# Kernel tuning notes

Hardware: AMD Instinct MI355X
Metric: run time of the kernel (lower is better)

Reference implementation:

```python
import jax, jax.numpy as jnp
import numpy as np

# Circuit geometry (matches QNN(sequence_length=16384, quantum_layer_quantity=4, output_quantity=64, entangler='basic'))
SEQ_LEN = 16384
N_ADDR = 14                      # ceil(log2(16384))
N_DATA = 4                       # UNIQUE_NUCLEOTIDE_QUANTITY
N_WIRES = N_ADDR + N_DATA        # 18
DIM = 2 ** N_WIRES               # 262144
N_LAYERS = 4
OUT = 64
BATCH = 32


def _apply_rx(state, theta, w):
    """Apply RX(theta) on wire w (wire 0 = most significant bit)."""
    c = jnp.cos(theta / 2).astype(jnp.complex64)
    s = (-1j * jnp.sin(theta / 2)).astype(jnp.complex64)
    U = jnp.stack([jnp.stack([c, s]), jnp.stack([s, c])])  # [2,2]
    B = state.shape[0]
    st = state.reshape(B, 2 ** w, 2, -1)
    st = jnp.einsum('ij,bajc->baic', U, st)
    return st.reshape(B, DIM)


def _apply_cnot(state, c, t):
    """CNOT with control wire c, target wire t."""
    B = state.shape[0]
    st = state.reshape((B,) + (2,) * N_WIRES)
    c_ax, t_ax = 1 + c, 1 + t
    p0 = jnp.take(st, 0, axis=c_ax)
    p1 = jnp.take(st, 1, axis=c_ax)
    t_ax_r = t_ax - 1 if t_ax > c_ax else t_ax
    p1 = jnp.flip(p1, axis=t_ax_r)  # X on target within control=1 block
    st = jnp.stack([p0, p1], axis=c_ax)
    return st.reshape(B, DIM)


def _circuit_probs(x, qweights):
    # Encoding: address register stays |0...0>, so among all multi-controlled
    # BasisEmbeddings only index 0 (control pattern all zeros) applies its X
    # gates. Resulting basis state index = bits of x[:,0,:] on the 4 data
    # wires (least-significant bits), address bits = 0.
    bits = x[:, 0, :]  # [B, 4]
    pw = jnp.asarray([8, 4, 2, 1], dtype=jnp.int32)
    idx = jnp.sum(bits * pw, axis=-1)  # [B]
    state = jax.nn.one_hot(idx, DIM, dtype=jnp.complex64)  # [B, DIM]
    # BasicEntanglerLayers: per layer, RX on every wire then a CNOT ring.
    for l in range(N_LAYERS):
        for w in range(N_WIRES):
            state = _apply_rx(state, qweights[l, w], w)
        for w in range(N_WIRES):
            state = _apply_cnot(state, w, (w + 1) % N_WIRES)
    return jnp.abs(state) ** 2  # qml.probs over all wires -> [B, DIM] float32


def setup_inputs() -> dict:
    key = jax.random.key(0)
    kx, kw, kW = jax.random.split(key, 3)
    x = jax.random.randint(kx, (BATCH, SEQ_LEN, N_DATA), 0, 2, dtype=jnp.int32)
    qweights = jax.random.uniform(kw, (N_LAYERS, N_WIRES), dtype=jnp.float32,
                                  maxval=2.0 * np.pi)
    W = jax.random.normal(kW, (OUT, DIM), dtype=jnp.float32) / np.sqrt(DIM)
    b = jnp.zeros((OUT,), dtype=jnp.float32)
    return {"x": x, "qweights": qweights, "W": W, "b": b}


def reference(x, qweights, W, b):
    probs = _circuit_probs(x, qweights)          # [B, 2^18]
    logits = probs @ W.T + b                     # [B, 64]
    return jax.nn.sigmoid(logits)
```

## Files before the change

kernel.cpp:

```cpp
#include <hip/hip_runtime.h>
#include <math.h>


#define DIM (1 << 18)
#define NW 18
#define CH 128
#define CPB 2
#define NMM (DIM / (CH * CPB))

#define PAD16(i) ((i) + ((i) >> 4))

typedef short short8 __attribute__((ext_vector_type(8)));
typedef float f32x4  __attribute__((ext_vector_type(4)));

__device__ __forceinline__ unsigned perm18(unsigned i) {
    unsigned s = i;
    s ^= s >> 1; s ^= s >> 2; s ^= s >> 4; s ^= s >> 8; s ^= s >> 16;
    unsigned out = s & 0x1FFFFu;
    out |= ((s ^ (i >> 17)) & 1u) << 17;
    return out;
}

__device__ __forceinline__ unsigned pinv18(unsigned b) {
    unsigned t = b & 0x1FFFFu;
    unsigned u = (t ^ (t >> 1)) & 0xFFFFu;
    unsigned i17 = ((b >> 17) ^ t) & 1u;
    unsigned i16 = ((t >> 16) ^ i17) & 1u;
    return u | (i16 << 16) | (i17 << 17);
}

__device__ __forceinline__ void bfly(float2& a0, float2& a1, float c, float s) {
    float2 n0 = make_float2(c * a0.x + s * a1.y, c * a0.y - s * a1.x);
    float2 n1 = make_float2(c * a1.x + s * a0.y, c * a1.y - s * a0.x);
    a0 = n0; a1 = n1;
}

__device__ __forceinline__ short f2bf(float x) {
    unsigned u = __float_as_uint(x);
    return (short)((u + 0x7FFFu + ((u >> 16) & 1u)) >> 16);
}

template<int R>
__device__ __forceinline__ void ldsRound(float2* t, int m, const float2* gsh) {
    constexpr int B = 1 << (2 * R);
    int low = m & (B - 1);
    int high = m >> (2 * R);
    int ib = (high << (2 * R + 2)) | low;
    int p00 = PAD16(ib), p01 = PAD16(ib | B), p10 = PAD16(ib | (2 * B)), p11 = PAD16(ib | (3 * B));
    float2 e00 = t[p00], e01 = t[p01], e10 = t[p10], e11 = t[p11];
    float2 g0 = gsh[2 * R], g1 = gsh[2 * R + 1];
    bfly(e00, e01, g0.x, g0.y);
    bfly(e10, e11, g0.x, g0.y);
    bfly(e00, e10, g1.x, g1.y);
    bfly(e01, e11, g1.x, g1.y);
    t[p00] = e00; t[p01] = e01; t[p10] = e10; t[p11] = e11;
}

__global__ __launch_bounds__(256) void kInit(float2* buf, const float* qw) {
    __shared__ float2 t[1088];
    __shared__ float2 gsh[10];
    int tid = threadIdx.x;
    if (tid < 10) {
        float th = qw[1 * NW + (17 - tid)] * 0.5f;
        gsh[tid] = make_float2(cosf(th), sinf(th));
    }
    float c[NW], s[NW];
#pragma unroll
    for (int w = 0; w < NW; ++w) {
        float th = qw[w] * 0.5f;
        c[w] = cosf(th); s[w] = sinf(th);
    }
    unsigned base = blockIdx.x * 1024u;
    float2 e[4];
#pragma unroll
    for (int b = 0; b < 4; ++b) {
        unsigned i = pinv18(base + 4 * tid + b);
        float m = 1.0f;
#pragma unroll
        for (int p = 0; p < 18; ++p)
            m *= ((i >> p) & 1u) ? s[17 - p] : c[17 - p];
        int k4 = __popc(i) & 3;
        if      (k4 == 0) e[b] = make_float2( m, 0.f);
        else if (k4 == 1) e[b] = make_float2(0.f, -m);
        else if (k4 == 2) e[b] = make_float2(-m, 0.f);
        else              e[b] = make_float2(0.f,  m);
    }
    __syncthreads();
    bfly(e[0], e[1], gsh[0].x, gsh[0].y);
    bfly(e[2], e[3], gsh[0].x, gsh[0].y);
    bfly(e[0], e[2], gsh[1].x, gsh[1].y);
    bfly(e[1], e[3], gsh[1].x, gsh[1].y);
    int ib = 4 * tid;
    t[PAD16(ib)] = e[0]; t[PAD16(ib + 1)] = e[1]; t[PAD16(ib + 2)] = e[2]; t[PAD16(ib + 3)] = e[3];
    __syncthreads();
    ldsRound<1>(t, tid, gsh); __syncthreads();
    ldsRound<2>(t, tid, gsh); __syncthreads();
    ldsRound<3>(t, tid, gsh); __syncthreads();
    float2 f00 = t[PAD16(tid)], f01 = t[PAD16(tid + 256)];
    float2 f10 = t[PAD16(tid + 512)], f11 = t[PAD16(tid + 768)];
    bfly(f00, f01, gsh[8].x, gsh[8].y);
    bfly(f10, f11, gsh[8].x, gsh[8].y);
    bfly(f00, f10, gsh[9].x, gsh[9].y);
    bfly(f01, f11, gsh[9].x, gsh[9].y);
    buf[base + tid] = f00; buf[base + tid + 256] = f01;
    buf[base + tid + 512] = f10; buf[base + tid + 768] = f11;
}

__global__ __launch_bounds__(256) void kA(float2* buf, const float* qw, int layer) {
    __shared__ float2 t[1088];
    __shared__ float2 gsh[10];
    int tid = threadIdx.x;
    if (tid < 10) {
        float th = qw[layer * NW + (17 - tid)] * 0.5f;
        gsh[tid] = make_float2(cosf(th), sinf(th));
    }
    unsigned base = blockIdx.x * 1024u;
    float2 e0 = buf[base + 4 * tid + 0];
    float2 e1 = buf[base + 4 * tid + 1];
    float2 e2 = buf[base + 4 * tid + 2];
    float2 e3 = buf[base + 4 * tid + 3];
    __syncthreads();
    bfly(e0, e1, gsh[0].x, gsh[0].y);
    bfly(e2, e3, gsh[0].x, gsh[0].y);
    bfly(e0, e2, gsh[1].x, gsh[1].y);
    bfly(e1, e3, gsh[1].x, gsh[1].y);
    int ib = 4 * tid;
    t[PAD16(ib)] = e0; t[PAD16(ib + 1)] = e1; t[PAD16(ib + 2)] = e2; t[PAD16(ib + 3)] = e3;
    __syncthreads();
    ldsRound<1>(t, tid, gsh); __syncthreads();
    ldsRound<2>(t, tid, gsh); __syncthreads();
    ldsRound<3>(t, tid, gsh); __syncthreads();
    float2 f00 = t[PAD16(tid)], f01 = t[PAD16(tid + 256)];
    float2 f10 = t[PAD16(tid + 512)], f11 = t[PAD16(tid + 768)];
    bfly(f00, f01, gsh[8].x, gsh[8].y);
    bfly(f10, f11, gsh[8].x, gsh[8].y);
    bfly(f00, f10, gsh[9].x, gsh[9].y);
    bfly(f01, f11, gsh[9].x, gsh[9].y);
    buf[base + tid] = f00; buf[base + tid + 256] = f01;
    buf[base + tid + 512] = f10; buf[base + tid + 768] = f11;
}

__global__ __launch_bounds__(256) void kBC(const float2* __restrict__ in, float2* out,
                                           float* probs, const float* qw, int layer) {
    __shared__ float2 t[1088];
    __shared__ float2 gsh[8];
    int tid = threadIdx.x;
    if (tid < 8) {
        float th = qw[layer * NW + (7 - tid)] * 0.5f;
        gsh[tid] = make_float2(cosf(th), sinf(th));
    }
    unsigned mblk = blockIdx.x;
    int mh = tid >> 2, lo = tid & 3;
    unsigned ibase = (mblk << 2) | lo;
    float2 e0 = in[((unsigned)(4 * mh + 0) << 10) | ibase];
    float2 e1 = in[((unsigned)(4 * mh + 1) << 10) | ibase];
    float2 e2 = in[((unsigned)(4 * mh + 2) << 10) | ibase];
    float2 e3 = in[((unsigned)(4 * mh + 3) << 10) | ibase];
    __syncthreads();
    bfly(e0, e1, gsh[0].x, gsh[0].y);
    bfly(e2, e3, gsh[0].x, gsh[0].y);
    bfly(e0, e2, gsh[1].x, gsh[1].y);
    bfly(e1, e3, gsh[1].x, gsh[1].y);
    {
        int k = 4 * (4 * mh) + lo;
        t[PAD16(k)] = e0; t[PAD16(k + 4)] = e1; t[PAD16(k + 8)] = e2; t[PAD16(k + 12)] = e3;
    }
    __syncthreads();
    {
        int hb = ((mh >> 2) << 4) | (mh & 3);
        int k00 = 4 * hb + lo, k01 = 4 * (hb | 4) + lo, k10 = 4 * (hb | 8) + lo, k11 = 4 * (hb | 12) + lo;
        int p00 = PAD16(k00), p01 = PAD16(k01), p10 = PAD16(k10), p11 = PAD16(k11);
        float2 a0 = t[p00], a1 = t[p01], a2 = t[p10], a3 = t[p11];
        bfly(a0, a1, gsh[2].x, gsh[2].y);
        bfly(a2, a3, gsh[2].x, gsh[2].y);
        bfly(a0, a2, gsh[3].x, gsh[3].y);
        bfly(a1, a3, gsh[3].x, gsh[3].y);
        t[p00] = a0; t[p01] = a1; t[p10] = a2; t[p11] = a3;
    }
    __syncthreads();
    {
        int hb = ((mh >> 4) << 6) | (mh & 15);
        int k00 = 4 * hb + lo, k01 = 4 * (hb | 16) + lo, k10 = 4 * (hb | 32) + lo, k11 = 4 * (hb | 48) + lo;
        int p00 = PAD16(k00), p01 = PAD16(k01), p10 = PAD16(k10), p11 = PAD16(k11);
        float2 a0 = t[p00], a1 = t[p01], a2 = t[p10], a3 = t[p11];
        bfly(a0, a1, gsh[4].x, gsh[4].y);
        bfly(a2, a3, gsh[4].x, gsh[4].y);
        bfly(a0, a2, gsh[5].x, gsh[5].y);
        bfly(a1, a3, gsh[5].x, gsh[5].y);
        t[p00] = a0; t[p01] = a1; t[p10] = a2; t[p11] = a3;
    }
    __syncthreads();
    {
        int k = 4 * mh + lo;
        float2 a0 = t[PAD16(k)], a1 = t[PAD16(k + 256)], a2 = t[PAD16(k + 512)], a3 = t[PAD16(k + 768)];
        bfly(a0, a1, gsh[6].x, gsh[6].y);
        bfly(a2, a3, gsh[6].x, gsh[6].y);
        bfly(a0, a2, gsh[7].x, gsh[7].y);
        bfly(a1, a3, gsh[7].x, gsh[7].y);
        unsigned i0 = ((unsigned)(mh +   0) << 10) | ibase;
        unsigned i1 = ((unsigned)(mh +  64) << 10) | ibase;
        unsigned i2 = ((unsigned)(mh + 128) << 10) | ibase;
        unsigned i3 = ((unsigned)(mh + 192) << 10) | ibase;
        if (probs) {
            probs[perm18(i0)] = a0.x * a0.x + a0.y * a0.y;
            probs[perm18(i1)] = a1.x * a1.x + a1.y * a1.y;
            probs[perm18(i2)] = a2.x * a2.x + a2.y * a2.y;
            probs[perm18(i3)] = a3.x * a3.x + a3.y * a3.y;
        } else {
            out[perm18(i0)] = a0;
            out[perm18(i1)] = a1;
            out[perm18(i2)] = a2;
            out[perm18(i3)] = a3;
        }
    }
}

__global__ __launch_bounds__(256) void k_mm(const float* __restrict__ p0,
                                            const float* __restrict__ W,
                                            float* __restrict__ partial) {
    __shared__ short Wl[64][136];
    __shared__ short Pl[16][136];
    __shared__ unsigned Tsh[16];
    int tid = threadIdx.x;
    if (tid < 16) {
        unsigned v = (unsigned)tid;
#pragma unroll
        for (int r = 0; r < 4; ++r) v = perm18(v);
        Tsh[tid] = v;
    }
    __syncthreads();

    unsigned d00 = (unsigned)blockIdx.x * (CH * CPB);
    int wrow = tid >> 5;
    int wcol = (tid & 31) * 4;
    int prow = tid >> 7;
    int pcol = tid & 127;
    unsigned Tp[8];
#pragma unroll
    for (int t = 0; t < 8; ++t) Tp[t] = Tsh[prow + 2 * t];

    int lane = tid & 63, wv = tid >> 6;
    f32x4 acc = {0.f, 0.f, 0.f, 0.f};

    float4 wr[8];
    float  pr[8];

#pragma unroll
    for (int t = 0; t < 8; ++t)
        wr[t] = *(const float4*)&W[(size_t)(wrow + 8 * t) * DIM + d00 + wcol];
#pragma unroll
    for (int t = 0; t < 8; ++t)
        pr[t] = p0[(d00 ^ (Tp[t] & ~127u)) + pcol];
#pragma unroll
    for (int t = 0; t < 8; ++t) {
        short4 b = make_short4(f2bf(wr[t].x), f2bf(wr[t].y), f2bf(wr[t].z), f2bf(wr[t].w));
        *(short4*)&Wl[wrow + 8 * t][wcol] = b;
    }
#pragma unroll
    for (int t = 0; t < 8; ++t)
        Pl[prow + 2 * t][pcol ^ (Tp[t] & 127u)] = f2bf(pr[t]);
    __syncthreads();

    {
        unsigned d1 = d00 + CH;
#pragma unroll
        for (int t = 0; t < 8; ++t)
            wr[t] = *(const float4*)&W[(size_t)(wrow + 8 * t) * DIM + d1 + wcol];
#pragma unroll
        for (int t = 0; t < 8; ++t)
            pr[t] = p0[(d1 ^ (Tp[t] & ~127u)) + pcol];
    }

    int arow = lane & 15, kg = (lane >> 4) * 8;
#pragma unroll
    for (int kk = 0; kk < 4; ++kk) {
        short8 a = *(const short8*)&Pl[arow][kk * 32 + kg];
        short8 b = *(const short8*)&Wl[16 * wv + arow][kk * 32 + kg];
        acc = __builtin_amdgcn_mfma_f32_16x16x32_bf16(a, b, acc, 0, 0, 0);
    }
    __syncthreads();

#pragma unroll
    for (int t = 0; t < 8; ++t) {
        short4 b = make_short4(f2bf(wr[t].x), f2bf(wr[t].y), f2bf(wr[t].z), f2bf(wr[t].w));
        *(short4*)&Wl[wrow + 8 * t][wcol] = b;
    }
#pragma unroll
    for (int t = 0; t < 8; ++t)
        Pl[prow + 2 * t][pcol ^ (Tp[t] & 127u)] = f2bf(pr[t]);
    __syncthreads();

#pragma unroll
    for (int kk = 0; kk < 4; ++kk) {
        short8 a = *(const short8*)&Pl[arow][kk * 32 + kg];
        short8 b = *(const short8*)&Wl[16 * wv + arow][kk * 32 + kg];
        acc = __builtin_amdgcn_mfma_f32_16x16x32_bf16(a, b, acc, 0, 0, 0);
    }

    float* dst = partial + (size_t)blockIdx.x * 1024;
#pragma unroll
    for (int r = 0; r < 4; ++r) {
        int jrow = (lane >> 4) * 4 + r;
        dst[jrow * 64 + 16 * wv + (lane & 15)] = acc[r];
    }
}

__global__ __launch_bounds__(256) void k_finalize(const float* __restrict__ partial,
                                                  const float* __restrict__ bias,
                                                  const int* __restrict__ x,
                                                  float* __restrict__ out) {
    int b = blockIdx.x;
    int tid = threadIdx.x;
    int ji = tid & 15, ci = tid >> 4;
    int jo = b * 16 + ji;
    float sum = 0.f;
#pragma unroll 8
    for (int c = ci; c < NMM; c += 16)
        sum += partial[(size_t)c * 1024 + jo];
    __shared__ float red[16][17];
    __shared__ float lg[16];
    __shared__ int sidx[32];
    red[ci][ji] = sum;
    if (tid < 32) {
        const int* xb = x + (size_t)tid * (16384 * 4);
        sidx[tid] = 8 * xb[0] + 4 * xb[1] + 2 * xb[2] + xb[3];
    }
    __syncthreads();
    if (ci == 0) {
        float s = 0.f;
#pragma unroll
        for (int k = 0; k < 16; ++k) s += red[k][ji];
        lg[ji] = s + bias[jo & 63];
    }
    __syncthreads();
    int myidx = b >> 2, o0 = (b & 3) * 16;
#pragma unroll
    for (int r = 0; r < 2; ++r) {
        int slot = tid + 256 * r;
        int bb = slot >> 4, k = slot & 15;
        if (sidx[bb] == myidx) {
            float z = lg[k];
            out[bb * 64 + o0 + k] = 1.f / (1.f + expf(-z));
        }
    }
}

extern "C" void kernel_launch(void* const* d_in, const int* in_sizes, int n_in,
                              void* d_out, int out_size, void* d_ws, size_t ws_size,
                              hipStream_t stream) {
    const int*   x    = (const int*)d_in[0];
    const float* qw   = (const float*)d_in[1];
    const float* W    = (const float*)d_in[2];
    const float* bias = (const float*)d_in[3];
    float* out = (float*)d_out;

    char* ws = (char*)d_ws;
    float2*   buf0    = (float2*)(ws + (1ull << 20));
    float2*   buf1    = (float2*)(ws + (4ull << 20));
    float*    probs   = (float*)(ws + (8ull << 20));
    float*    partial = (float*)(ws + (16ull << 20));

    kInit<<<256, 256, 0, stream>>>(buf0, qw);
    kBC  <<<256, 256, 0, stream>>>(buf0, buf1, nullptr, qw, 1);
    kA   <<<256, 256, 0, stream>>>(buf1, qw, 2);
    kBC  <<<256, 256, 0, stream>>>(buf1, buf0, nullptr, qw, 2);
    kA   <<<256, 256, 0, stream>>>(buf0, qw, 3);
    kBC  <<<256, 256, 0, stream>>>(buf0, nullptr, probs, qw, 3);

    k_mm<<<NMM, 256, 0, stream>>>(probs, W, partial);
    k_finalize<<<64, 256, 0, stream>>>(partial, bias, x, out);
}
```

Before: 57.39 us.

## Repartition state-vector butterfly passes and lengthen matmul chunk loop

Changes how qubit wires are split between the A and B/C passes. The A kernels now handle wires 0 and 17 plus the wires selected by the block index, and perform the CNOT-ring permutation while gathering into shared memory. The B/C kernel becomes an in-place pass with plain strided stores, and the probability scatter through perm18 happens only in the last pass. The matmul kernel now processes 4 chunks per block in a prefetch loop instead of 2, which halves the block count and the partial-sum traffic but leaves fewer blocks to fill the GPU.

```diff
diff --git a/kernel.cpp b/kernel.cpp
--- a/kernel.cpp
+++ b/kernel.cpp
@@ -5,7 +5,7 @@
 #define DIM (1 << 18)
 #define NW 18
 #define CH 128
-#define CPB 2
+#define CPB 4
 #define NMM (DIM / (CH * CPB))
 
 #define PAD16(i) ((i) + ((i) >> 4))
@@ -29,6 +29,11 @@
     return u | (i16 << 16) | (i17 << 17);
 }
 
+__device__ __forceinline__ unsigned ginv9(unsigned x) {
+    x ^= x >> 1; x ^= x >> 2; x ^= x >> 4; x ^= x >> 8;
+    return x & 511u;
+}
+
 __device__ __forceinline__ void bfly(float2& a0, float2& a1, float c, float s) {
     float2 n0 = make_float2(c * a0.x + s * a1.y, c * a0.y - s * a1.x);
     float2 n1 = make_float2(c * a1.x + s * a0.y, c * a1.y - s * a0.x);
@@ -40,15 +45,14 @@
     return (short)((u + 0x7FFFu + ((u >> 16) & 1u)) >> 16);
 }
 
-template<int R>
-__device__ __forceinline__ void ldsRound(float2* t, int m, const float2* gsh) {
-    constexpr int B = 1 << (2 * R);
+template<int RB>
+__device__ __forceinline__ void slotRound(float2* t, int m, float2 g0, float2 g1) {
+    constexpr int B = 1 << RB;
     int low = m & (B - 1);
-    int high = m >> (2 * R);
-    int ib = (high << (2 * R + 2)) | low;
-    int p00 = PAD16(ib), p01 = PAD16(ib | B), p10 = PAD16(ib | (2 * B)), p11 = PAD16(ib | (3 * B));
+    int high = m >> RB;
+    int ib = (high << (RB + 2)) | low;
+    int p00 = PAD16(ib), p01 = PAD16(ib | B), p10 = PAD16(ib | 2 * B), p11 = PAD16(ib | 3 * B);
     float2 e00 = t[p00], e01 = t[p01], e10 = t[p10], e11 = t[p11];
-    float2 g0 = gsh[2 * R], g1 = gsh[2 * R + 1];
     bfly(e00, e01, g0.x, g0.y);
     bfly(e10, e11, g0.x, g0.y);
     bfly(e00, e10, g1.x, g1.y);
@@ -56,12 +60,30 @@
     t[p00] = e00; t[p01] = e01; t[p10] = e10; t[p11] = e11;
 }
 
-__global__ __launch_bounds__(256) void kInit(float2* buf, const float* qw) {
+__device__ __forceinline__ void kaTail(float2* t, int tid, const float2* gsh,
+                                       float2* __restrict__ out, unsigned B9) {
+    slotRound<1>(t, tid, gsh[1], gsh[2]); __syncthreads();
+    slotRound<3>(t, tid, gsh[3], gsh[4]); __syncthreads();
+    slotRound<5>(t, tid, gsh[5], gsh[6]); __syncthreads();
+    int low = tid & 127, high = tid >> 7;
+    int ib = (high << 9) | low;
+    float2 a0 = t[PAD16(ib)], a1 = t[PAD16(ib | 128)];
+    float2 a2 = t[PAD16(ib | 256)], a3 = t[PAD16(ib | 384)];
+    bfly(a0, a1, gsh[7].x, gsh[7].y);
+    bfly(a2, a3, gsh[7].x, gsh[7].y);
+    bfly(a0, a2, gsh[8].x, gsh[8].y);
+    bfly(a1, a3, gsh[8].x, gsh[8].y);
+    unsigned ob = ((unsigned)high << 17) | (B9 << 9) | (unsigned)low;
+    out[ob] = a0; out[ob + 128] = a1; out[ob + 256] = a2; out[ob + 384] = a3;
+}
+
+__global__ __launch_bounds__(256) void kInit(float2* __restrict__ out, const float* qw) {
     __shared__ float2 t[1088];
     __shared__ float2 gsh[10];
     int tid = threadIdx.x;
     if (tid < 10) {
-        float th = qw[1 * NW + (17 - tid)] * 0.5f;
+        int p = (tid == 9) ? 17 : tid;
+        float th = qw[1 * NW + (17 - p)] * 0.5f;
         gsh[tid] = make_float2(cosf(th), sinf(th));
     }
     float c[NW], s[NW];
@@ -70,97 +92,105 @@
         float th = qw[w] * 0.5f;
         c[w] = cosf(th); s[w] = sinf(th);
     }
-    unsigned base = blockIdx.x * 1024u;
-    float2 e[4];
-#pragma unroll
-    for (int b = 0; b < 4; ++b) {
-        unsigned i = pinv18(base + 4 * tid + b);
-        float m = 1.0f;
-#pragma unroll
-        for (int p = 0; p < 18; ++p)
-            m *= ((i >> p) & 1u) ? s[17 - p] : c[17 - p];
-        int k4 = __popc(i) & 3;
-        if      (k4 == 0) e[b] = make_float2( m, 0.f);
-        else if (k4 == 1) e[b] = make_float2(0.f, -m);
-        else if (k4 == 2) e[b] = make_float2(-m, 0.f);
-        else              e[b] = make_float2(0.f,  m);
-    }
-    __syncthreads();
-    bfly(e[0], e[1], gsh[0].x, gsh[0].y);
-    bfly(e[2], e[3], gsh[0].x, gsh[0].y);
-    bfly(e[0], e[2], gsh[1].x, gsh[1].y);
-    bfly(e[1], e[3], gsh[1].x, gsh[1].y);
-    int ib = 4 * tid;
-    t[PAD16(ib)] = e[0]; t[PAD16(ib + 1)] = e[1]; t[PAD16(ib + 2)] = e[2]; t[PAD16(ib + 3)] = e[3];
-    __syncthreads();
-    ldsRound<1>(t, tid, gsh); __syncthreads();
-    ldsRound<2>(t, tid, gsh); __syncthreads();
-    ldsRound<3>(t, tid, gsh); __syncthreads();
-    float2 f00 = t[PAD16(tid)], f01 = t[PAD16(tid + 256)];
-    float2 f10 = t[PAD16(tid + 512)], f11 = t[PAD16(tid + 768)];
-    bfly(f00, f01, gsh[8].x, gsh[8].y);
-    bfly(f10, f11, gsh[8].x, gsh[8].y);
-    bfly(f00, f10, gsh[9].x, gsh[9].y);
-    bfly(f01, f11, gsh[9].x, gsh[9].y);
-    buf[base + tid] = f00; buf[base + tid + 256] = f01;
-    buf[base + tid + 512] = f10; buf[base + tid + 768] = f11;
-}
-
-__global__ __launch_bounds__(256) void kA(float2* buf, const float* qw, int layer) {
+    unsigned B9 = blockIdx.x;
+    float2 e[2][2];
+#pragma unroll
+    for (int p17 = 0; p17 < 2; ++p17)
+#pragma unroll
+        for (int b0 = 0; b0 < 2; ++b0) {
+            unsigned b = ((unsigned)p17 << 17) | (B9 << 9) | ((unsigned)tid << 1) | (unsigned)b0;
+            unsigned i = pinv18(b);
+            float m = 1.0f;
+#pragma unroll
+            for (int p = 0; p < 18; ++p)
+                m *= ((i >> p) & 1u) ? s[17 - p] : c[17 - p];
+            int k4 = __popc(i) & 3;
+            if      (k4 == 0) e[p17][b0] = make_float2( m, 0.f);
+            else if (k4 == 1) e[p17][b0] = make_float2(0.f, -m);
+            else if (k4 == 2) e[p17][b0] = make_float2(-m, 0.f);
+            else              e[p17][b0] = make_float2(0.f,  m);
+        }
+    __syncthreads();
+    bfly(e[0][0], e[0][1], gsh[0].x, gsh[0].y);
+    bfly(e[1][0], e[1][1], gsh[0].x, gsh[0].y);
+    bfly(e[0][0], e[1][0], gsh[9].x, gsh[9].y);
+    bfly(e[0][1], e[1][1], gsh[9].x, gsh[9].y);
+    int sb = tid << 1;
+    t[PAD16(sb)] = e[0][0];       t[PAD16(sb | 1)] = e[0][1];
+    t[PAD16(sb | 512)] = e[1][0]; t[PAD16(sb | 513)] = e[1][1];
+    __syncthreads();
+    kaTail(t, tid, gsh, out, B9);
+}
+
+__global__ __launch_bounds__(256) void kA(const float2* __restrict__ in,
+                                          float2* __restrict__ out,
+                                          const float* qw, int layer) {
     __shared__ float2 t[1088];
     __shared__ float2 gsh[10];
     int tid = threadIdx.x;
     if (tid < 10) {
-        float th = qw[layer * NW + (17 - tid)] * 0.5f;
+        int p = (tid == 9) ? 17 : tid;
+        float th = qw[layer * NW + (17 - p)] * 0.5f;
         gsh[tid] = make_float2(cosf(th), sinf(th));
     }
-    unsigned base = blockIdx.x * 1024u;
-    float2 e0 = buf[base + 4 * tid + 0];
-    float2 e1 = buf[base + 4 * tid + 1];
-    float2 e2 = buf[base + 4 * tid + 2];
-    float2 e3 = buf[base + 4 * tid + 3];
+    unsigned B9 = blockIdx.x;
+    unsigned C = pinv18(B9 << 9);
+    unsigned c9 = C & 511u;
+    unsigned base0 = C & ~511u;
+    unsigned base1 = base0 ^ 0x30000u;
+    float2 v[2][2];
+#pragma unroll
+    for (int ee = 0; ee < 2; ++ee)
+#pragma unroll
+        for (int r = 0; r < 2; ++r)
+            v[ee][r] = in[(ee ? base1 : base0) + (unsigned)tid + 256u * r];
+#pragma unroll
+    for (int ee = 0; ee < 2; ++ee)
+#pragma unroll
+        for (int r = 0; r < 2; ++r) {
+            unsigned k = (unsigned)tid + 256u * r;
+            unsigned x = (k ^ c9) & 511u;
+            unsigned bl = ginv9(x);
+            unsigned p17 = ((unsigned)__popc(x) ^ (unsigned)ee) & 1u;
+            t[PAD16((p17 << 9) | bl)] = v[ee][r];
+        }
+    __syncthreads();
+    {
+        int s00 = tid << 1;
+        int p00 = PAD16(s00), p01 = PAD16(s00 | 1), p10 = PAD16(s00 | 512), p11 = PAD16(s00 | 513);
+        float2 e00 = t[p00], e01 = t[p01], e10 = t[p10], e11 = t[p11];
+        bfly(e00, e01, gsh[0].x, gsh[0].y);
+        bfly(e10, e11, gsh[0].x, gsh[0].y);
+        bfly(e00, e10, gsh[9].x, gsh[9].y);
+        bfly(e01, e11, gsh[9].x, gsh[9].y);
+        t[p00] = e00; t[p01] = e01; t[p10] = e10; t[p11] = e11;
+    }
+    __syncthreads();
+    kaTail(t, tid, gsh, out, B9);
+}
+
+__global__ __launch_bounds__(256) void kBC(float2* __restrict__ buf, float* probs,
+                                           const float* qw, int layer) {
+    __shared__ float2 t[1088];
+    __shared__ float2 gsh[8];
+    int tid = threadIdx.x;
+    if (tid < 8) {
+        float th = qw[layer * NW + (8 - tid)] * 0.5f;
+        gsh[tid] = make_float2(cosf(th), sinf(th));
+    }
+    unsigned blk = blockIdx.x;
+    unsigned ibase = ((blk >> 7) << 17) | ((blk & 127u) << 2) | 0u;
+    int mh = tid >> 2, lo = tid & 3;
+    ibase |= (unsigned)lo;
+    float2 e0 = buf[((unsigned)(4 * mh + 0) << 9) | ibase];
+    float2 e1 = buf[((unsigned)(4 * mh + 1) << 9) | ibase];
+    float2 e2 = buf[((unsigned)(4 * mh + 2) << 9) | ibase];
+    float2 e3 = buf[((unsigned)(4 * mh + 3) << 9) | ibase];
     __syncthreads();
     bfly(e0, e1, gsh[0].x, gsh[0].y);
     bfly(e2, e3, gsh[0].x, gsh[0].y);
     bfly(e0, e2, gsh[1].x, gsh[1].y);
     bfly(e1, e3, gsh[1].x, gsh[1].y);
-    int ib = 4 * tid;
-    t[PAD16(ib)] = e0; t[PAD16(ib + 1)] = e1; t[PAD16(ib + 2)] = e2; t[PAD16(ib + 3)] = e3;
-    __syncthreads();
-    ldsRound<1>(t, tid, gsh); __syncthreads();
-    ldsRound<2>(t, tid, gsh); __syncthreads();
-    ldsRound<3>(t, tid, gsh); __syncthreads();
-    float2 f00 = t[PAD16(tid)], f01 = t[PAD16(tid + 256)];
-    float2 f10 = t[PAD16(tid + 512)], f11 = t[PAD16(tid + 768)];
-    bfly(f00, f01, gsh[8].x, gsh[8].y);
-    bfly(f10, f11, gsh[8].x, gsh[8].y);
-    bfly(f00, f10, gsh[9].x, gsh[9].y);
-    bfly(f01, f11, gsh[9].x, gsh[9].y);
-    buf[base + tid] = f00; buf[base + tid + 256] = f01;
-    buf[base + tid + 512] = f10; buf[base + tid + 768] = f11;
-}
-
-__global__ __launch_bounds__(256) void kBC(const float2* __restrict__ in, float2* out,
-                                           float* probs, const float* qw, int layer) {
-    __shared__ float2 t[1088];
-    __shared__ float2 gsh[8];
-    int tid = threadIdx.x;
-    if (tid < 8) {
-        float th = qw[layer * NW + (7 - tid)] * 0.5f;
-        gsh[tid] = make_float2(cosf(th), sinf(th));
-    }
-    unsigned mblk = blockIdx.x;
-    int mh = tid >> 2, lo = tid & 3;
-    unsigned ibase = (mblk << 2) | lo;
-    float2 e0 = in[((unsigned)(4 * mh + 0) << 10) | ibase];
-    float2 e1 = in[((unsigned)(4 * mh + 1) << 10) | ibase];
-    float2 e2 = in[((unsigned)(4 * mh + 2) << 10) | ibase];
-    float2 e3 = in[((unsigned)(4 * mh + 3) << 10) | ibase];
-    __syncthreads();
-    bfly(e0, e1, gsh[0].x, gsh[0].y);
-    bfly(e2, e3, gsh[0].x, gsh[0].y);
-    bfly(e0, e2, gsh[1].x, gsh[1].y);
-    bfly(e1, e3, gsh[1].x, gsh[1].y);
     {
         int k = 4 * (4 * mh) + lo;
         t[PAD16(k)] = e0; t[PAD16(k + 4)] = e1; t[PAD16(k + 8)] = e2; t[PAD16(k + 12)] = e3;
@@ -168,8 +198,8 @@
     __syncthreads();
     {
         int hb = ((mh >> 2) << 4) | (mh & 3);
-        int k00 = 4 * hb + lo, k01 = 4 * (hb | 4) + lo, k10 = 4 * (hb | 8) + lo, k11 = 4 * (hb | 12) + lo;
-        int p00 = PAD16(k00), p01 = PAD16(k01), p10 = PAD16(k10), p11 = PAD16(k11);
+        int p00 = PAD16(4 * hb + lo), p01 = PAD16(4 * (hb | 4) + lo);
+        int p10 = PAD16(4 * (hb | 8) + lo), p11 = PAD16(4 * (hb | 12) + lo);
         float2 a0 = t[p00], a1 = t[p01], a2 = t[p10], a3 = t[p11];
         bfly(a0, a1, gsh[2].x, gsh[2].y);
         bfly(a2, a3, gsh[2].x, gsh[2].y);
@@ -180,8 +210,8 @@
     __syncthreads();
     {
         int hb = ((mh >> 4) << 6) | (mh & 15);
-        int k00 = 4 * hb + lo, k01 = 4 * (hb | 16) + lo, k10 = 4 * (hb | 32) + lo, k11 = 4 * (hb | 48) + lo;
-        int p00 = PAD16(k00), p01 = PAD16(k01), p10 = PAD16(k10), p11 = PAD16(k11);
+        int p00 = PAD16(4 * hb + lo), p01 = PAD16(4 * (hb | 16) + lo);
+        int p10 = PAD16(4 * (hb | 32) + lo), p11 = PAD16(4 * (hb | 48) + lo);
         float2 a0 = t[p00], a1 = t[p01], a2 = t[p10], a3 = t[p11];
         bfly(a0, a1, gsh[4].x, gsh[4].y);
         bfly(a2, a3, gsh[4].x, gsh[4].y);
@@ -197,20 +227,17 @@
         bfly(a2, a3, gsh[6].x, gsh[6].y);
         bfly(a0, a2, gsh[7].x, gsh[7].y);
         bfly(a1, a3, gsh[7].x, gsh[7].y);
-        unsigned i0 = ((unsigned)(mh +   0) << 10) | ibase;
-        unsigned i1 = ((unsigned)(mh +  64) << 10) | ibase;
-        unsigned i2 = ((unsigned)(mh + 128) << 10) | ibase;
-        unsigned i3 = ((unsigned)(mh + 192) << 10) | ibase;
+        unsigned i0 = ((unsigned)(mh +   0) << 9) | ibase;
+        unsigned i1 = ((unsigned)(mh +  64) << 9) | ibase;
+        unsigned i2 = ((unsigned)(mh + 128) << 9) | ibase;
+        unsigned i3 = ((unsigned)(mh + 192) << 9) | ibase;
         if (probs) {
             probs[perm18(i0)] = a0.x * a0.x + a0.y * a0.y;
             probs[perm18(i1)] = a1.x * a1.x + a1.y * a1.y;
             probs[perm18(i2)] = a2.x * a2.x + a2.y * a2.y;
             probs[perm18(i3)] = a3.x * a3.x + a3.y * a3.y;
         } else {
-            out[perm18(i0)] = a0;
-            out[perm18(i1)] = a1;
-            out[perm18(i2)] = a2;
-            out[perm18(i3)] = a3;
+            buf[i0] = a0; buf[i1] = a1; buf[i2] = a2; buf[i3] = a3;
         }
     }
 }
@@ -240,6 +267,7 @@
     for (int t = 0; t < 8; ++t) Tp[t] = Tsh[prow + 2 * t];
 
     int lane = tid & 63, wv = tid >> 6;
+    int arow = lane & 15, kg = (lane >> 4) * 8;
     f32x4 acc = {0.f, 0.f, 0.f, 0.f};
 
     float4 wr[8];
@@ -261,40 +289,34 @@
         Pl[prow + 2 * t][pcol ^ (Tp[t] & 127u)] = f2bf(pr[t]);
     __syncthreads();
 
-    {
-        unsigned d1 = d00 + CH;
-#pragma unroll
-        for (int t = 0; t < 8; ++t)
-            wr[t] = *(const float4*)&W[(size_t)(wrow + 8 * t) * DIM + d1 + wcol];
-#pragma unroll
-        for (int t = 0; t < 8; ++t)
-            pr[t] = p0[(d1 ^ (Tp[t] & ~127u)) + pcol];
-    }
-
-    int arow = lane & 15, kg = (lane >> 4) * 8;
-#pragma unroll
-    for (int kk = 0; kk < 4; ++kk) {
-        short8 a = *(const short8*)&Pl[arow][kk * 32 + kg];
-        short8 b = *(const short8*)&Wl[16 * wv + arow][kk * 32 + kg];
-        acc = __builtin_amdgcn_mfma_f32_16x16x32_bf16(a, b, acc, 0, 0, 0);
-    }
-    __syncthreads();
-
-#pragma unroll
-    for (int t = 0; t < 8; ++t) {
-        short4 b = make_short4(f2bf(wr[t].x), f2bf(wr[t].y), f2bf(wr[t].z), f2bf(wr[t].w));
-        *(short4*)&Wl[wrow + 8 * t][wcol] = b;
-    }
-#pragma unroll
-    for (int t = 0; t < 8; ++t)
-        Pl[prow + 2 * t][pcol ^ (Tp[t] & 127u)] = f2bf(pr[t]);
-    __syncthreads();
-
-#pragma unroll
-    for (int kk = 0; kk < 4; ++kk) {
-        short8 a = *(const short8*)&Pl[arow][kk * 32 + kg];
-        short8 b = *(const short8*)&Wl[16 * wv + arow][kk * 32 + kg];
-        acc = __builtin_amdgcn_mfma_f32_16x16x32_bf16(a, b, acc, 0, 0, 0);
+    for (int cc = 0; cc < CPB; ++cc) {
+        if (cc + 1 < CPB) {
+            unsigned d1 = d00 + (unsigned)(cc + 1) * CH;
+#pragma unroll
+            for (int t = 0; t < 8; ++t)
+                wr[t] = *(const float4*)&W[(size_t)(wrow + 8 * t) * DIM + d1 + wcol];
+#pragma unroll
+            for (int t = 0; t < 8; ++t)
+                pr[t] = p0[(d1 ^ (Tp[t] & ~127u)) + pcol];
+        }
+#pragma unroll
+        for (int kk = 0; kk < 4; ++kk) {
+            short8 a = *(const short8*)&Pl[arow][kk * 32 + kg];
+            short8 b = *(const short8*)&Wl[16 * wv + arow][kk * 32 + kg];
+            acc = __builtin_amdgcn_mfma_f32_16x16x32_bf16(a, b, acc, 0, 0, 0);
+        }
+        __syncthreads();
+        if (cc + 1 < CPB) {
+#pragma unroll
+            for (int t = 0; t < 8; ++t) {
+                short4 b = make_short4(f2bf(wr[t].x), f2bf(wr[t].y), f2bf(wr[t].z), f2bf(wr[t].w));
+                *(short4*)&Wl[wrow + 8 * t][wcol] = b;
+            }
+#pragma unroll
+            for (int t = 0; t < 8; ++t)
+                Pl[prow + 2 * t][pcol ^ (Tp[t] & 127u)] = f2bf(pr[t]);
+            __syncthreads();
+        }
     }
 
     float* dst = partial + (size_t)blockIdx.x * 1024;
@@ -361,11 +383,11 @@
     float*    partial = (float*)(ws + (16ull << 20));
 
     kInit<<<256, 256, 0, stream>>>(buf0, qw);
-    kBC  <<<256, 256, 0, stream>>>(buf0, buf1, nullptr, qw, 1);
-    kA   <<<256, 256, 0, stream>>>(buf1, qw, 2);
-    kBC  <<<256, 256, 0, stream>>>(buf1, buf0, nullptr, qw, 2);
-    kA   <<<256, 256, 0, stream>>>(buf0, qw, 3);
-    kBC  <<<256, 256, 0, stream>>>(buf0, nullptr, probs, qw, 3);
+    kBC  <<<256, 256, 0, stream>>>(buf0, nullptr, qw, 1);
+    kA   <<<256, 256, 0, stream>>>(buf0, buf1, qw, 2);
+    kBC  <<<256, 256, 0, stream>>>(buf1, nullptr, qw, 2);
+    kA   <<<256, 256, 0, stream>>>(buf1, buf0, qw, 3);
+    kBC  <<<256, 256, 0, stream>>>(buf0, probs, qw, 3);
 
     k_mm<<<NMM, 256, 0, stream>>>(probs, W, partial);
     k_finalize<<<64, 256, 0, stream>>>(partial, bias, x, out);
```

Result: no change. 56.30 us (-1.9%).
